# Kernel optimization log

Hardware: AMD Instinct MI355X
Metric: run time of the kernel (lower is better)

## Reference

```python
import jax, jax.numpy as jnp
import numpy as np

N, E, DIN, DH, DOUT, H, G = 50000, 640000, 128, 64, 64, 4, 16

_PARAM_SHAPES = {
    "gat1_W": (DIN, H * DH), "gat1_asrc": (H, DH), "gat1_adst": (H, DH), "gat1_b": (DH,),
    "gat2_W": (DH, H * DH), "gat2_asrc": (H, DH), "gat2_adst": (H, DH), "gat2_b": (DH,),
    "gin_W1": (DH, DH), "gin_b1": (DH,), "gin_W2": (DH, DH), "gin_b2": (DH,),
    "sage1_Wl": (DH, DH), "sage1_bl": (DH,), "sage1_Wr": (DH, DH),
    "sage2_Wl": (DH, DH), "sage2_bl": (DH,), "sage2_Wr": (DH, DH),
    "tr_Wq": (DH, H * DH), "tr_bq": (H * DH,), "tr_Wk": (DH, H * DH), "tr_bk": (H * DH,),
    "tr_Wv": (DH, H * DH), "tr_bv": (H * DH,), "tr_Ws": (DH, DH), "tr_bs": (DH,),
    "ec_W1": (2 * DH, DH), "ec_b1": (DH,), "ec_W2": (DH, DH), "ec_b2": (DH,),
    "fc1_W": (DH, DH), "fc1_b": (DH,), "fc2_W": (DH, DOUT), "fc2_b": (DOUT,),
}
_PARAM_NAMES = list(_PARAM_SHAPES)


def setup_inputs() -> dict:
    key = jax.random.key(0)
    inp = {}
    inp["x"] = jax.random.normal(jax.random.fold_in(key, 0), (N, DIN), jnp.float32)
    inp["edge_index"] = jax.random.randint(jax.random.fold_in(key, 1), (2, E), 0, N, dtype=jnp.int32)
    inp["batch"] = jnp.sort(jax.random.randint(jax.random.fold_in(key, 2), (N,), 0, G, dtype=jnp.int32))
    for i, (name, shp) in enumerate(_PARAM_SHAPES.items()):
        inp[name] = jax.random.normal(jax.random.fold_in(key, 10 + i), shp, jnp.float32) * 0.05
    return inp


def _edge_softmax(logit, dst, n):
    # softmax over incoming edges of each target node (PyG scatter-softmax)
    m = jax.ops.segment_max(logit, dst, num_segments=n)
    e = jnp.exp(logit - m[dst])
    z = jax.ops.segment_sum(e, dst, num_segments=n)
    return e / (z[dst] + 1e-16)


def _forward(x, src, dst, batch, p):
    relu = jax.nn.relu
    # GATConv adds self-loops by default
    loop = jnp.arange(N, dtype=src.dtype)
    src_sl = jnp.concatenate([src, loop])
    dst_sl = jnp.concatenate([dst, loop])

    def gat(h_in, W, a_s, a_d, b):
        h = (h_in @ W).reshape(N, H, DH)                    # [N,H,D]
        ls = jnp.einsum('nhd,hd->nh', h, a_s)
        ld = jnp.einsum('nhd,hd->nh', h, a_d)
        logit = jax.nn.leaky_relu(ls[src_sl] + ld[dst_sl], 0.2)   # [E+N,H]
        alpha = _edge_softmax(logit, dst_sl, N)
        out = jax.ops.segment_sum(h[src_sl] * alpha[:, :, None], dst_sl, num_segments=N)
        return out.mean(axis=1) + b                          # concat=False -> head mean + bias

    x1 = relu(gat(x, p["gat1_W"], p["gat1_asrc"], p["gat1_adst"], p["gat1_b"]))
    x2 = relu(gat(x1, p["gat2_W"], p["gat2_asrc"], p["gat2_adst"], p["gat2_b"]))

    # GINConv: nn((1+eps)*x + sum_j x_j), eps=0
    agg = jax.ops.segment_sum(x2[src], dst, num_segments=N)
    x3 = relu(relu((x2 + agg) @ p["gin_W1"] + p["gin_b1"]) @ p["gin_W2"] + p["gin_b2"])

    deg = jax.ops.segment_sum(jnp.ones((E,), x.dtype), dst, num_segments=N)
    deg = jnp.maximum(deg, 1.0)[:, None]

    def sage(h_in, Wl, bl, Wr):
        mean = jax.ops.segment_sum(h_in[src], dst, num_segments=N) / deg
        return mean @ Wl + bl + h_in @ Wr

    xs = relu(sage(x3, p["sage1_Wl"], p["sage1_bl"], p["sage1_Wr"]))
    x4 = relu(sage(xs, p["sage2_Wl"], p["sage2_bl"], p["sage2_Wr"]))

    # TransformerConv (heads=4, concat=False, root_weight skip)
    q = (x4 @ p["tr_Wq"] + p["tr_bq"]).reshape(N, H, DH)
    k = (x4 @ p["tr_Wk"] + p["tr_bk"]).reshape(N, H, DH)
    v = (x4 @ p["tr_Wv"] + p["tr_bv"]).reshape(N, H, DH)
    logit = (q[dst] * k[src]).sum(-1) * (1.0 / np.sqrt(DH))  # [E,H]
    alpha = _edge_softmax(logit, dst, N)
    tout = jax.ops.segment_sum(v[src] * alpha[:, :, None], dst, num_segments=N).mean(axis=1)
    x5 = relu(tout + x4 @ p["tr_Ws"] + p["tr_bs"])

    # EdgeConv: max_j nn([x_i, x_j - x_i])
    xi = x5[dst]
    feat = jnp.concatenate([xi, x5[src] - xi], axis=1)       # [E, 2*DH]
    msg = relu(feat @ p["ec_W1"] + p["ec_b1"]) @ p["ec_W2"] + p["ec_b2"]
    emax = jax.ops.segment_max(msg, dst, num_segments=N)
    x6 = relu(jnp.where(jnp.isfinite(emax), emax, 0.0))      # isolated nodes -> 0

    # global_mean_pool over batch ids
    cnt = jax.ops.segment_sum(jnp.ones((N,), x.dtype), batch, num_segments=G)
    gmean = jax.ops.segment_sum(x6, batch, num_segments=G) / jnp.maximum(cnt, 1.0)[:, None]

    # dropout layers are identity in eval mode
    return relu(gmean @ p["fc1_W"] + p["fc1_b"]) @ p["fc2_W"] + p["fc2_b"]


def reference(x, edge_index, batch,
              gat1_W, gat1_asrc, gat1_adst, gat1_b,
              gat2_W, gat2_asrc, gat2_adst, gat2_b,
              gin_W1, gin_b1, gin_W2, gin_b2,
              sage1_Wl, sage1_bl, sage1_Wr,
              sage2_Wl, sage2_bl, sage2_Wr,
              tr_Wq, tr_bq, tr_Wk, tr_bk, tr_Wv, tr_bv, tr_Ws, tr_bs,
              ec_W1, ec_b1, ec_W2, ec_b2,
              fc1_W, fc1_b, fc2_W, fc2_b):
    L = dict(locals())
    p = {n: L[n] for n in _PARAM_NAMES}
    return _forward(x, edge_index[0], edge_index[1], batch, p)
```

## Files before the change

kernel.cpp:

```cpp
#include <hip/hip_runtime.h>

#define NN 50000
#define EE 640000
#define GG 16
#define N64 (NN*64)

static inline int cdiv(int a,int b){return (a+b-1)/b;}

typedef __attribute__((ext_vector_type(8))) short bfrag;
typedef __attribute__((ext_vector_type(4))) float ffrag;

__device__ __forceinline__ float lrelu(float x){ return x>0.f? x : 0.2f*x; }
__device__ __forceinline__ unsigned fenc(float f){
  unsigned u=__float_as_uint(f);
  return (u&0x80000000u)? ~u : (u|0x80000000u);
}
__device__ __forceinline__ float bf2f(unsigned short u){ return __uint_as_float(((unsigned)u)<<16); }
__device__ __forceinline__ unsigned short f2bf(float f){
  unsigned u=__float_as_uint(f);
  u += 0x7FFFu + ((u>>16)&1u);
  return (unsigned short)(u>>16);
}

__global__ void zero_kernel(unsigned* p, int n){
  int i=blockIdx.x*blockDim.x+threadIdx.x;
  if(i<n) p[i]=0u;
}

__global__ void hist_kernel(const int* __restrict__ dst, int* __restrict__ cnt){
  int e=blockIdx.x*blockDim.x+threadIdx.x;
  if(e<EE) atomicAdd(&cnt[dst[e]],1);
}

__global__ __launch_bounds__(1024) void scan1_kernel(const int* __restrict__ cnt,
    int* __restrict__ rowptr, int* __restrict__ bsum){
  __shared__ int wsum[16];
  int t=threadIdx.x, b=blockIdx.x;
  int i=b*1024+t;
  int v=(i<NN)?cnt[i]:0;
  int lane=t&63, w=t>>6;
  int inc=v;
  #pragma unroll
  for(int o=1;o<64;o<<=1){ int u=__shfl_up(inc,o,64); if(lane>=o) inc+=u; }
  if(lane==63) wsum[w]=inc;
  __syncthreads();
  if(t<16){
    int s=wsum[t];
    #pragma unroll
    for(int o=1;o<16;o<<=1){ int u=__shfl_up(s,o,16); if(t>=o) s+=u; }
    wsum[t]=s;
  }
  __syncthreads();
  int woff=(w>0)?wsum[w-1]:0;
  if(i<NN) rowptr[i]=woff+inc-v;
  if(t==1023) bsum[b]=wsum[15];
}

__global__ void scan2_kernel(const int* __restrict__ bsum, int* __restrict__ boff, int* __restrict__ rowptr, int nb){
  int t=threadIdx.x;
  int v=(t<nb)?bsum[t]:0;
  int inc=v;
  #pragma unroll
  for(int o=1;o<64;o<<=1){ int u=__shfl_up(inc,o,64); if(t>=o) inc+=u; }
  if(t<nb) boff[t]=inc-v;
  if(t==63) rowptr[NN]=inc;
}

__global__ void scan3_kernel(int* __restrict__ rowptr, const int* __restrict__ boff,
                             const int* __restrict__ cnt, float* __restrict__ invdeg){
  int i=blockIdx.x*blockDim.x+threadIdx.x;
  if(i<NN){
    rowptr[i]+=boff[i>>10];
    invdeg[i]=1.f/fmaxf((float)cnt[i],1.f);
  }
}

__global__ void fill_kernel(const int* __restrict__ src, const int* __restrict__ dst,
                            const int* __restrict__ rowptr, int* __restrict__ fillp,
                            int* __restrict__ srcS, int* __restrict__ dstS){
  int e=blockIdx.x*blockDim.x+threadIdx.x;
  if(e>=EE) return;
  int d=dst[e];
  int p=rowptr[d]+atomicAdd(&fillp[d],1);
  srcS[p]=src[e]; dstS[p]=d;
}

__global__ void cvtx_kernel(const float* __restrict__ x, unsigned short* __restrict__ xb){
  int i=blockIdx.x*blockDim.x+threadIdx.x;
  if(i>=NN*32) return;
  float4 v=*(const float4*)(x+(size_t)i*4);
  ushort4 o; o.x=f2bf(v.x); o.y=f2bf(v.y); o.z=f2bf(v.z); o.w=f2bf(v.w);
  *(ushort4*)(xb+(size_t)i*4)=o;
}

__global__ void prep_kernel(
    const float* __restrict__ g1W, const float* __restrict__ g2W,
    const float* __restrict__ giW1, const float* __restrict__ giW2,
    const float* __restrict__ s1Wl, const float* __restrict__ s1Wr,
    const float* __restrict__ s2Wl, const float* __restrict__ s2Wr,
    const float* __restrict__ Wq, const float* __restrict__ Wk,
    const float* __restrict__ Wv, const float* __restrict__ Ws,
    const float* __restrict__ ecW1, const float* __restrict__ ecW2,
    const float* __restrict__ bq, const float* __restrict__ bk, const float* __restrict__ eb1,
    unsigned short* __restrict__ wt, float* __restrict__ bqk, float* __restrict__ bPQ){
  int i=blockIdx.x*blockDim.x+threadIdx.x;
  if(i<32768){ int n=i>>7,k=i&127; wt[i]=f2bf(g1W[k*256+n]); return; } i-=32768;
  if(i<16384){ int n=i>>6,k=i&63; wt[32768+i]=f2bf(g2W[k*256+n]); return; } i-=16384;
  if(i<4096){ int n=i>>6,k=i&63; wt[49152+i]=f2bf(giW1[k*64+n]); return; } i-=4096;
  if(i<4096){ int n=i>>6,k=i&63; wt[53248+i]=f2bf(giW2[k*64+n]); return; } i-=4096;
  if(i<8192){ int n=i>>7,k=i&127; float v=(k<64)?s1Wl[k*64+n]:s1Wr[(k-64)*64+n];
              wt[57344+i]=f2bf(v); return; } i-=8192;
  if(i<8192){ int n=i>>7,k=i&127; float v=(k<64)?s2Wl[k*64+n]:s2Wr[(k-64)*64+n];
              wt[65536+i]=f2bf(v); return; } i-=8192;
  if(i<32768){ int n=i>>6,k=i&63; float v=(n<256)?Wq[k*256+n]:Wk[k*256+(n-256)];
               wt[73728+i]=f2bf(v); return; } i-=32768;
  if(i<16384){ int n=i>>6,k=i&63; wt[106496+i]=f2bf(Wv[k*256+n]); return; } i-=16384;
  if(i<4096){ int n=i>>6,k=i&63; wt[122880+i]=f2bf(Ws[k*64+n]); return; } i-=4096;
  if(i<8192){ int n=i>>6,k=i&63;
              float v=(n<64)?(ecW1[k*64+n]-ecW1[(64+k)*64+n]):ecW1[(64+k)*64+(n-64)];
              wt[126976+i]=f2bf(v); return; } i-=8192;
  if(i<4096){ int n=i>>6,k=i&63; wt[135168+i]=f2bf(ecW2[k*64+n]); return; } i-=4096;
  if(i<640){
    if(i<256) bqk[i]=bq[i];
    else if(i<512) bqk[i]=bk[i-256];
    else { int j=i-512; bPQ[j]=(j<64)?eb1[j]:0.f; }
  }
}

template<int K>
__global__ __launch_bounds__(256) void mgemm_kernel(
    const unsigned short* __restrict__ A, const unsigned short* __restrict__ Wt,
    const float* __restrict__ bias,
    float* __restrict__ Cf, unsigned short* __restrict__ Cb, int ldc, int relu_flag,
    const float* __restrict__ a_s, const float* __restrict__ a_d,
    float* __restrict__ lsO, float* __restrict__ ldO){
  __shared__ float lsP[2][4][64];
  const int m0=blockIdx.x*64;
  const int tid=threadIdx.x;
  const int w=tid>>6, l=tid&63, lo=l&15, quad=l>>4;
  const int colg=blockIdx.y*64 + w*16 + lo;
  const unsigned short* wrow=Wt+(size_t)colg*K+quad*8;
  ffrag acc[4];
  #pragma unroll
  for(int t=0;t<4;t++) acc[t]=(ffrag){0.f,0.f,0.f,0.f};
  int rows[4];
  #pragma unroll
  for(int t=0;t<4;t++){ int r=m0+t*16+lo; rows[t]=(r<NN)?r:(NN-1); }
  #pragma unroll
  for(int kc=0;kc<K;kc+=32){
    bfrag b=*(const bfrag*)(wrow+kc);
    #pragma unroll
    for(int t=0;t<4;t++){
      bfrag a=*(const bfrag*)(A+(size_t)rows[t]*K+kc+quad*8);
      acc[t]=__builtin_amdgcn_mfma_f32_16x16x32_bf16(a,b,acc[t],0,0,0);
    }
  }
  float bv=bias?bias[colg]:0.f;
  float asv=0.f,adv=0.f;
  if(lsO){ asv=a_s[colg]; adv=a_d[colg]; }
  #pragma unroll
  for(int t=0;t<4;t++){
    #pragma unroll
    for(int r=0;r<4;r++){
      float v=acc[t][r]+bv;
      if(relu_flag) v=fmaxf(v,0.f);
      int row=m0+t*16+quad*4+r;
      if(row<NN){
        if(Cb) Cb[(size_t)row*ldc+colg]=f2bf(v);
        else   Cf[(size_t)row*ldc+colg]=v;
      }
      if(lsO){
        float ps=v*asv, pd=v*adv;
        #pragma unroll
        for(int o=1;o<16;o<<=1){ ps+=__shfl_xor(ps,o,16); pd+=__shfl_xor(pd,o,16); }
        if(lo==0){ int lr=t*16+quad*4+r; lsP[0][w][lr]=ps; lsP[1][w][lr]=pd; }
      }
    }
  }
  if(lsO){
    __syncthreads();
    if(tid<64){
      int row=m0+tid;
      if(row<NN){
        lsO[(size_t)row*4+blockIdx.y]=lsP[0][0][tid]+lsP[0][1][tid]+lsP[0][2][tid]+lsP[0][3][tid];
        ldO[(size_t)row*4+blockIdx.y]=lsP[1][0][tid]+lsP[1][1][tid]+lsP[1][2][tid]+lsP[1][3][tid];
      }
    }
  }
}

__global__ void gat_exp_kernel(const int* __restrict__ srcS, const int* __restrict__ dstS,
    const float* __restrict__ ls4, const float* __restrict__ ld4, float* __restrict__ eE){
  int j=blockIdx.x*blockDim.x+threadIdx.x;
  if(j>=EE) return;
  int s=srcS[j], d=dstS[j];
  const float4 a=*(const float4*)(ls4+(size_t)4*s);
  const float4 b=*(const float4*)(ld4+(size_t)4*d);
  *(float4*)(eE+(size_t)4*j)=make_float4(
    __expf(lrelu(a.x+b.x)),__expf(lrelu(a.y+b.y)),
    __expf(lrelu(a.z+b.z)),__expf(lrelu(a.w+b.w)));
}

__global__ __launch_bounds__(256) void gat1p_kernel(const unsigned short* __restrict__ h,
    const int* __restrict__ rowptr, const int* __restrict__ srcS,
    const float* __restrict__ eE,
    const float* __restrict__ ls4, const float* __restrict__ ld4,
    const float* __restrict__ bias, unsigned short* __restrict__ outb){
  __shared__ float cz[4][4];
  __shared__ float ca[4][4][64];
  int w=threadIdx.x>>6, lane=threadIdx.x&63;
  int n=blockIdx.x*2+(w>>1);
  int half=w&1;
  float z0=0.f,z1=0.f,z2=0.f,z3=0.f;
  float a0=0.f,a1=0.f,a2=0.f,a3=0.f;
  if(n<NN){
    int r0=rowptr[n], r1=rowptr[n+1];
    int mid=(r0+r1)>>1;
    if(half==0){
      const float4 ldv=*(const float4*)(ld4+(size_t)4*n);
      const float4 lsv=*(const float4*)(ls4+(size_t)4*n);
      z0=__expf(lrelu(lsv.x+ldv.x)); z1=__expf(lrelu(lsv.y+ldv.y));
      z2=__expf(lrelu(lsv.z+ldv.z)); z3=__expf(lrelu(lsv.w+ldv.w));
      const unsigned short* hn=h+(size_t)n*256;
      a0=z0*bf2f(hn[lane]); a1=z1*bf2f(hn[64+lane]);
      a2=z2*bf2f(hn[128+lane]); a3=z3*bf2f(hn[192+lane]);
    }
    int j = half? mid : r0;
    int je= half? r1  : mid;
    for(; j+3<je; j+=4){
      int s0=srcS[j], s1=srcS[j+1], s2=srcS[j+2], s3=srcS[j+3];
      const float4 E0=*(const float4*)(eE+(size_t)4*j);
      const float4 E1=*(const float4*)(eE+(size_t)4*(j+1));
      const float4 E2=*(const float4*)(eE+(size_t)4*(j+2));
      const float4 E3=*(const float4*)(eE+(size_t)4*(j+3));
      const unsigned short* h0=h+(size_t)s0*256;
      const unsigned short* h1=h+(size_t)s1*256;
      const unsigned short* h2=h+(size_t)s2*256;
      const unsigned short* h3=h+(size_t)s3*256;
      z0+=(E0.x+E1.x)+(E2.x+E3.x); z1+=(E0.y+E1.y)+(E2.y+E3.y);
      z2+=(E0.z+E1.z)+(E2.z+E3.z); z3+=(E0.w+E1.w)+(E2.w+E3.w);
      a0+=(E0.x*bf2f(h0[lane])+E1.x*bf2f(h1[lane]))+(E2.x*bf2f(h2[lane])+E3.x*bf2f(h3[lane]));
      a1+=(E0.y*bf2f(h0[64+lane])+E1.y*bf2f(h1[64+lane]))+(E2.y*bf2f(h2[64+lane])+E3.y*bf2f(h3[64+lane]));
      a2+=(E0.z*bf2f(h0[128+lane])+E1.z*bf2f(h1[128+lane]))+(E2.z*bf2f(h2[128+lane])+E3.z*bf2f(h3[128+lane]));
      a3+=(E0.w*bf2f(h0[192+lane])+E1.w*bf2f(h1[192+lane]))+(E2.w*bf2f(h2[192+lane])+E3.w*bf2f(h3[192+lane]));
    }
    for(; j<je; j++){
      int s0=srcS[j];
      const float4 E0=*(const float4*)(eE+(size_t)4*j);
      const unsigned short* h0=h+(size_t)s0*256;
      z0+=E0.x; z1+=E0.y; z2+=E0.z; z3+=E0.w;
      a0+=E0.x*bf2f(h0[lane]); a1+=E0.y*bf2f(h0[64+lane]);
      a2+=E0.z*bf2f(h0[128+lane]); a3+=E0.w*bf2f(h0[192+lane]);
    }
  }
  if(lane==0){ cz[w][0]=z0; cz[w][1]=z1; cz[w][2]=z2; cz[w][3]=z3; }
  ca[w][0][lane]=a0; ca[w][1][lane]=a1; ca[w][2][lane]=a2; ca[w][3][lane]=a3;
  __syncthreads();
  if(threadIdx.x<128){
    int ni=threadIdx.x>>6, l=threadIdx.x&63;
    int n2=blockIdx.x*2+ni;
    if(n2<NN){
      int w0=ni*2, w1=w0+1;
      float Z0=cz[w0][0]+cz[w1][0], Z1=cz[w0][1]+cz[w1][1];
      float Z2=cz[w0][2]+cz[w1][2], Z3=cz[w0][3]+cz[w1][3];
      float A0=ca[w0][0][l]+ca[w1][0][l], A1=ca[w0][1][l]+ca[w1][1][l];
      float A2=ca[w0][2][l]+ca[w1][2][l], A3=ca[w0][3][l]+ca[w1][3][l];
      float r=0.25f*(A0/(Z0+1e-16f)+A1/(Z1+1e-16f)+A2/(Z2+1e-16f)+A3/(Z3+1e-16f))+bias[l];
      outb[(size_t)n2*64+l]=f2bf(fmaxf(r,0.f));
    }
  }
}

__global__ __launch_bounds__(256) void agg_kernel(const unsigned short* __restrict__ xin,
    const int* __restrict__ rowptr, const int* __restrict__ srcS,
    unsigned short* __restrict__ out){
  int n=blockIdx.x*4+(threadIdx.x>>6);
  int lane=threadIdx.x&63;
  if(n>=NN) return;
  int r0=rowptr[n], r1=rowptr[n+1];
  float acc=bf2f(xin[(size_t)n*64+lane]);
  int j=r0;
  for(; j+3<r1; j+=4){
    int s0=srcS[j], s1=srcS[j+1], s2=srcS[j+2], s3=srcS[j+3];
    acc+=(bf2f(xin[(size_t)s0*64+lane])+bf2f(xin[(size_t)s1*64+lane]))
        +(bf2f(xin[(size_t)s2*64+lane])+bf2f(xin[(size_t)s3*64+lane]));
  }
  for(; j<r1; j++) acc+=bf2f(xin[(size_t)srcS[j]*64+lane]);
  out[(size_t)n*64+lane]=f2bf(acc);
}

__global__ __launch_bounds__(256) void agg2_kernel(const unsigned short* __restrict__ xin,
    const int* __restrict__ rowptr, const int* __restrict__ srcS,
    const float* __restrict__ invdeg, unsigned short* __restrict__ out128b){
  int n=blockIdx.x*4+(threadIdx.x>>6);
  int lane=threadIdx.x&63;
  if(n>=NN) return;
  int r0=rowptr[n], r1=rowptr[n+1];
  float acc=0.f;
  int j=r0;
  for(; j+3<r1; j+=4){
    int s0=srcS[j], s1=srcS[j+1], s2=srcS[j+2], s3=srcS[j+3];
    acc+=(bf2f(xin[(size_t)s0*64+lane])+bf2f(xin[(size_t)s1*64+lane]))
        +(bf2f(xin[(size_t)s2*64+lane])+bf2f(xin[(size_t)s3*64+lane]));
  }
  for(; j<r1; j++) acc+=bf2f(xin[(size_t)srcS[j]*64+lane]);
  out128b[(size_t)n*128+lane]=f2bf(acc*invdeg[n]);
  out128b[(size_t)n*128+64+lane]=xin[(size_t)n*64+lane];
}

__global__ __launch_bounds__(256) void tr_pass1_kernel(const int* __restrict__ srcS, const int* __restrict__ dstS,
    const unsigned short* __restrict__ qk, float* __restrict__ lg){
  int e=blockIdx.x*16+(threadIdx.x>>4);
  int t=threadIdx.x&15;
  if(e>=EE) return;
  int s=srcS[e], d=dstS[e];
  const unsigned short* qd=qk+(size_t)d*512+t*4;
  const unsigned short* ks=qk+(size_t)s*512+256+t*4;
  ushort4 ku0=*(const ushort4*)(ks);
  ushort4 ku1=*(const ushort4*)(ks+64);
  ushort4 ku2=*(const ushort4*)(ks+128);
  ushort4 ku3=*(const ushort4*)(ks+192);
  ushort4 qu0=*(const ushort4*)(qd);
  ushort4 qu1=*(const ushort4*)(qd+64);
  ushort4 qu2=*(const ushort4*)(qd+128);
  ushort4 qu3=*(const ushort4*)(qd+192);
  float v0=bf2f(ku0.x)*bf2f(qu0.x)+bf2f(ku0.y)*bf2f(qu0.y)+bf2f(ku0.z)*bf2f(qu0.z)+bf2f(ku0.w)*bf2f(qu0.w);
  float v1=bf2f(ku1.x)*bf2f(qu1.x)+bf2f(ku1.y)*bf2f(qu1.y)+bf2f(ku1.z)*bf2f(qu1.z)+bf2f(ku1.w)*bf2f(qu1.w);
  float v2=bf2f(ku2.x)*bf2f(qu2.x)+bf2f(ku2.y)*bf2f(qu2.y)+bf2f(ku2.z)*bf2f(qu2.z)+bf2f(ku2.w)*bf2f(qu2.w);
  float v3=bf2f(ku3.x)*bf2f(qu3.x)+bf2f(ku3.y)*bf2f(qu3.y)+bf2f(ku3.z)*bf2f(qu3.z)+bf2f(ku3.w)*bf2f(qu3.w);
  #pragma unroll
  for(int o=1;o<16;o<<=1){
    v0+=__shfl_xor(v0,o,16); v1+=__shfl_xor(v1,o,16);
    v2+=__shfl_xor(v2,o,16); v3+=__shfl_xor(v3,o,16);
  }
  if(t==0)
    *(float4*)(lg+(size_t)4*e)=make_float4(__expf(v0*0.125f),__expf(v1*0.125f),
                                           __expf(v2*0.125f),__expf(v3*0.125f));
}

__global__ __launch_bounds__(256) void tr_pass2_kernel(const int* __restrict__ rowptr, const int* __restrict__ srcS,
    const float* __restrict__ lg,
    const unsigned short* __restrict__ v, const float* __restrict__ skip, unsigned short* __restrict__ x5b){
  __shared__ float cz[4][4];
  __shared__ float ca[4][4][64];
  int w=threadIdx.x>>6, lane=threadIdx.x&63;
  int n=blockIdx.x*2+(w>>1);
  int half=w&1;
  float z0=0.f,z1=0.f,z2=0.f,z3=0.f;
  float a0=0.f,a1=0.f,a2=0.f,a3=0.f;
  if(n<NN){
    int r0=rowptr[n], r1=rowptr[n+1];
    int mid=(r0+r1)>>1;
    int j = half? mid : r0;
    int je= half? r1  : mid;
    for(; j+3<je; j+=4){
      int s0=srcS[j], s1=srcS[j+1], s2=srcS[j+2], s3=srcS[j+3];
      const float4 E0=*(const float4*)(lg+(size_t)4*j);
      const float4 E1=*(const float4*)(lg+(size_t)4*(j+1));
      const float4 E2=*(const float4*)(lg+(size_t)4*(j+2));
      const float4 E3=*(const float4*)(lg+(size_t)4*(j+3));
      const unsigned short* v0=v+(size_t)s0*256;
      const unsigned short* v1=v+(size_t)s1*256;
      const unsigned short* v2=v+(size_t)s2*256;
      const unsigned short* v3=v+(size_t)s3*256;
      z0+=(E0.x+E1.x)+(E2.x+E3.x); z1+=(E0.y+E1.y)+(E2.y+E3.y);
      z2+=(E0.z+E1.z)+(E2.z+E3.z); z3+=(E0.w+E1.w)+(E2.w+E3.w);
      a0+=(E0.x*bf2f(v0[lane])+E1.x*bf2f(v1[lane]))+(E2.x*bf2f(v2[lane])+E3.x*bf2f(v3[lane]));
      a1+=(E0.y*bf2f(v0[64+lane])+E1.y*bf2f(v1[64+lane]))+(E2.y*bf2f(v2[64+lane])+E3.y*bf2f(v3[64+lane]));
      a2+=(E0.z*bf2f(v0[128+lane])+E1.z*bf2f(v1[128+lane]))+(E2.z*bf2f(v2[128+lane])+E3.z*bf2f(v3[128+lane]));
      a3+=(E0.w*bf2f(v0[192+lane])+E1.w*bf2f(v1[192+lane]))+(E2.w*bf2f(v2[192+lane])+E3.w*bf2f(v3[192+lane]));
    }
    for(; j<je; j++){
      int s0=srcS[j];
      const float4 E0=*(const float4*)(lg+(size_t)4*j);
      const unsigned short* v0=v+(size_t)s0*256;
      z0+=E0.x; z1+=E0.y; z2+=E0.z; z3+=E0.w;
      a0+=E0.x*bf2f(v0[lane]); a1+=E0.y*bf2f(v0[64+lane]);
      a2+=E0.z*bf2f(v0[128+lane]); a3+=E0.w*bf2f(v0[192+lane]);
    }
  }
  if(lane==0){ cz[w][0]=z0; cz[w][1]=z1; cz[w][2]=z2; cz[w][3]=z3; }
  ca[w][0][lane]=a0; ca[w][1][lane]=a1; ca[w][2][lane]=a2; ca[w][3][lane]=a3;
  __syncthreads();
  if(threadIdx.x<128){
    int ni=threadIdx.x>>6, l=threadIdx.x&63;
    int n2=blockIdx.x*2+ni;
    if(n2<NN){
      int w0=ni*2, w1=w0+1;
      float Z0=cz[w0][0]+cz[w1][0], Z1=cz[w0][1]+cz[w1][1];
      float Z2=cz[w0][2]+cz[w1][2], Z3=cz[w0][3]+cz[w1][3];
      float A0=ca[w0][0][l]+ca[w1][0][l], A1=ca[w0][1][l]+ca[w1][1][l];
      float A2=ca[w0][2][l]+ca[w1][2][l], A3=ca[w0][3][l]+ca[w1][3][l];
      float t=0.25f*(A0/(Z0+1e-16f)+A1/(Z1+1e-16f)+A2/(Z2+1e-16f)+A3/(Z3+1e-16f))+skip[(size_t)n2*64+l];
      x5b[(size_t)n2*64+l]=f2bf(fmaxf(t,0.f));
    }
  }
}

__global__ __launch_bounds__(256) void edgeconv3_kernel(
    const unsigned short* __restrict__ PQ,
    const int* __restrict__ srcS, const int* __restrict__ dstS,
    const unsigned short* __restrict__ W2t, const float* __restrict__ b2,
    unsigned* __restrict__ emax){
  __shared__ unsigned short Hs[64][72];
  __shared__ float As[64][66];
  __shared__ int dstL[64];
  const int e0=blockIdx.x*64;
  const int tid=threadIdx.x;
  if(tid<64) dstL[tid]=dstS[e0+tid];
  #pragma unroll
  for(int it=0;it<4;it++){
    int linear=it*1024+tid*4;
    int m=linear>>6, k=linear&63;
    int e=e0+m;
    int dn=dstS[e], sn=srcS[e];
    ushort4 pu=*(const ushort4*)(PQ+(size_t)dn*128+k);
    ushort4 qu=*(const ushort4*)(PQ+(size_t)sn*128+64+k);
    ushort4 hh;
    hh.x=f2bf(fmaxf(bf2f(pu.x)+bf2f(qu.x),0.f));
    hh.y=f2bf(fmaxf(bf2f(pu.y)+bf2f(qu.y),0.f));
    hh.z=f2bf(fmaxf(bf2f(pu.z)+bf2f(qu.z),0.f));
    hh.w=f2bf(fmaxf(bf2f(pu.w)+bf2f(qu.w),0.f));
    *(ushort4*)&Hs[m][k]=hh;
  }
  __syncthreads();
  const int w=tid>>6, l=tid&63, lo=l&15, quad=l>>4;
  const int colg=w*16+lo;
  ffrag acc[4];
  #pragma unroll
  for(int t=0;t<4;t++) acc[t]=(ffrag){0.f,0.f,0.f,0.f};
  #pragma unroll
  for(int kc=0;kc<64;kc+=32){
    bfrag b=*(const bfrag*)(W2t+(size_t)colg*64+kc+quad*8);
    #pragma unroll
    for(int t=0;t<4;t++){
      bfrag a=*(const bfrag*)(&Hs[t*16+lo][kc+quad*8]);
      acc[t]=__builtin_amdgcn_mfma_f32_16x16x32_bf16(a,b,acc[t],0,0,0);
    }
  }
  float bv=b2[colg];
  #pragma unroll
  for(int t=0;t<4;t++)
    #pragma unroll
    for(int r=0;r<4;r++)
      As[t*16+quad*4+r][colg]=acc[t][r]+bv;
  __syncthreads();
  if(tid<64){
    const int c=tid;
    const int dFirst=dstL[0], dLast=dstL[63];
    int dprev=dFirst;
    float mx=As[0][c];
    #pragma unroll 8
    for(int m=1;m<64;m++){
      int dn=dstL[m];
      float v=As[m][c];
      if(dn!=dprev){
        unsigned* addr=&emax[(size_t)dprev*64+c];
        unsigned enc=fenc(mx);
        if(dprev!=dFirst && dprev!=dLast) *addr=enc;
        else atomicMax(addr,enc);
        dprev=dn; mx=v;
      }else mx=fmaxf(mx,v);
    }
    unsigned* addr=&emax[(size_t)dprev*64+c];
    unsigned enc=fenc(mx);
    if(dprev!=dFirst && dprev!=dLast) *addr=enc;
    else atomicMax(addr,enc);
  }
}

__global__ __launch_bounds__(256) void pool_kernel(const unsigned* __restrict__ emax, const int* __restrict__ batch,
                                                   float* __restrict__ pooled){
  const int NB=200;
  int base=blockIdx.x*NB;
  int lane=threadIdx.x&63;
  int wsub=threadIdx.x>>6;
  float acc=0.f; int curg=-1;
  for(int idx=wsub; idx<NB; idx+=4){
    int n=base+idx;
    if(n>=NN) break;
    int g=batch[n];
    if(g!=curg){
      if(curg>=0) atomicAdd(&pooled[curg*64+lane],acc);
      acc=0.f; curg=g;
    }
    unsigned u=emax[(size_t)n*64+lane];
    acc+=(u>=0x80000000u)? __uint_as_float(u&0x7fffffffu) : 0.f;
  }
  if(curg>=0) atomicAdd(&pooled[curg*64+lane],acc);
}

__global__ __launch_bounds__(256) void final_kernel(const float* __restrict__ pooled, const int* __restrict__ batch,
    const float* __restrict__ fc1W, const float* __restrict__ fc1b,
    const float* __restrict__ fc2W, const float* __restrict__ fc2b,
    float* __restrict__ out){
  __shared__ float gm[16][64];
  __shared__ float t1[16][64];
  __shared__ int cgs[17];
  int t=threadIdx.x;
  if(t<17){
    int lo=0, hi=NN;
    while(lo<hi){ int mid=(lo+hi)>>1; if(batch[mid]<t) lo=mid+1; else hi=mid; }
    cgs[t]=lo;
  }
  __syncthreads();
  for(int r=0;r<4;r++){
    int idx=r*256+t; int g=idx>>6, d=idx&63;
    float c=(float)(cgs[g+1]-cgs[g]);
    gm[g][d]=pooled[idx]/fmaxf(c,1.f);
  }
  __syncthreads();
  for(int r=0;r<4;r++){
    int idx=r*256+t; int g=idx>>6, d=idx&63;
    float a=fc1b[d];
    for(int k2=0;k2<64;k2++) a+=gm[g][k2]*fc1W[k2*64+d];
    t1[g][d]=fmaxf(a,0.f);
  }
  __syncthreads();
  for(int r=0;r<4;r++){
    int idx=r*256+t; int g=idx>>6, d=idx&63;
    float a=fc2b[d];
    for(int k2=0;k2<64;k2++) a+=t1[g][k2]*fc2W[k2*64+d];
    out[idx]=a;
  }
}

extern "C" void kernel_launch(void* const* d_in, const int* in_sizes, int n_in,
                              void* d_out, int out_size, void* d_ws, size_t ws_size,
                              hipStream_t stream){
  const float* x       =(const float*)d_in[0];
  const int*   ei      =(const int*)  d_in[1];
  const int*   src     =ei;
  const int*   dst     =ei+EE;
  const int*   batch   =(const int*)  d_in[2];
  const float* gat1_W  =(const float*)d_in[3];
  const float* gat1_as =(const float*)d_in[4];
  const float* gat1_ad =(const float*)d_in[5];
  const float* gat1_b  =(const float*)d_in[6];
  const float* gat2_W  =(const float*)d_in[7];
  const float* gat2_as =(const float*)d_in[8];
  const float* gat2_ad =(const float*)d_in[9];
  const float* gat2_b  =(const float*)d_in[10];
  const float* gin_W1  =(const float*)d_in[11];
  const float* gin_b1  =(const float*)d_in[12];
  const float* gin_W2  =(const float*)d_in[13];
  const float* gin_b2  =(const float*)d_in[14];
  const float* sage1_Wl=(const float*)d_in[15];
  const float* sage1_bl=(const float*)d_in[16];
  const float* sage1_Wr=(const float*)d_in[17];
  const float* sage2_Wl=(const float*)d_in[18];
  const float* sage2_bl=(const float*)d_in[19];
  const float* sage2_Wr=(const float*)d_in[20];
  const float* tr_Wq   =(const float*)d_in[21];
  const float* tr_bq   =(const float*)d_in[22];
  const float* tr_Wk   =(const float*)d_in[23];
  const float* tr_bk   =(const float*)d_in[24];
  const float* tr_Wv   =(const float*)d_in[25];
  const float* tr_bv   =(const float*)d_in[26];
  const float* tr_Ws   =(const float*)d_in[27];
  const float* tr_bs   =(const float*)d_in[28];
  const float* ec_W1   =(const float*)d_in[29];
  const float* ec_b1   =(const float*)d_in[30];
  const float* ec_W2   =(const float*)d_in[31];
  const float* ec_b2   =(const float*)d_in[32];
  const float* fc1_W   =(const float*)d_in[33];
  const float* fc1_b   =(const float*)d_in[34];
  const float* fc2_W   =(const float*)d_in[35];
  const float* fc2_b   =(const float*)d_in[36];

  float* base=(float*)d_ws;
  size_t off=0;
  auto alloc=[&](size_t n){ float* p=base+off; off+=n; return p; };
  float* A_big =alloc((size_t)NN*256);
  float* nb0   =alloc(N64);
  float* nb1   =alloc(N64);
  float* nb2   =alloc(N64);
  float* nb3   =alloc(N64);
  float* nb4   =alloc(N64);
  float* nb5   =alloc(N64);
  float* logitE=alloc((size_t)EE*4);
  float* ls    =alloc(NN*4);
  float* ldb   =alloc(NN*4);
  float* invdeg=alloc(NN);
  float* pooled=alloc(GG*64);
  float* wbuf  =alloc(70000);
  float* bbuf  =alloc(640);
  int* ibase=(int*)(base+off);
  int* srcS  =ibase;
  int* dstS  =ibase+EE;
  int* cnt   =ibase+2*EE;
  int* fillp =ibase+2*EE+NN;
  int* rowptr=ibase+2*EE+2*NN;
  int* bsum  =ibase+2*EE+3*NN+8;
  int* boff  =bsum+64;

  const int BT=256;
  const int NSB=cdiv(NN,1024);
  zero_kernel<<<cdiv(2*NN,BT),BT,0,stream>>>((unsigned*)cnt,2*NN);
  zero_kernel<<<cdiv(GG*64,BT),BT,0,stream>>>((unsigned*)pooled,GG*64);
  zero_kernel<<<cdiv(N64,BT),BT,0,stream>>>((unsigned*)nb5,N64);
  hist_kernel<<<cdiv(EE,BT),BT,0,stream>>>(dst,cnt);
  scan1_kernel<<<NSB,1024,0,stream>>>(cnt,rowptr,bsum);
  scan2_kernel<<<1,64,0,stream>>>(bsum,boff,rowptr,NSB);
  scan3_kernel<<<cdiv(NN,BT),BT,0,stream>>>(rowptr,boff,cnt,invdeg);
  fill_kernel<<<cdiv(EE,BT),BT,0,stream>>>(src,dst,rowptr,fillp,srcS,dstS);

  const int GB=cdiv(NN,64);
  const int GW=cdiv(NN,4);
  const int GW2=cdiv(NN,2);

  unsigned short* wt =(unsigned short*)wbuf;
  float* bqk=bbuf;
  float* bPQ=bbuf+512;
  unsigned short* hbf  =(unsigned short*)A_big;
  unsigned short* xb   =(unsigned short*)A_big+(size_t)NN*256;
  unsigned short* xcatb=(unsigned short*)A_big;
  unsigned short* qkb  =(unsigned short*)A_big;
  unsigned short* x1b  =(unsigned short*)nb0;
  unsigned short* x2b  =(unsigned short*)nb1;
  unsigned short* tb   =(unsigned short*)nb2;
  unsigned short* hb3  =(unsigned short*)nb3;
  unsigned short* x3b  =(unsigned short*)nb1;
  unsigned short* xsb  =(unsigned short*)nb2;
  unsigned short* x4b  =(unsigned short*)nb0;
  unsigned short* vb   =(unsigned short*)nb1;
  unsigned short* x5b  =(unsigned short*)nb4;
  float* skipf=nb3;
  unsigned short* PQb  =(unsigned short*)nb1;

  prep_kernel<<<cdiv(139904,BT),BT,0,stream>>>(gat1_W,gat2_W,gin_W1,gin_W2,
      sage1_Wl,sage1_Wr,sage2_Wl,sage2_Wr,tr_Wq,tr_Wk,tr_Wv,tr_Ws,ec_W1,ec_W2,
      tr_bq,tr_bk,ec_b1,wt,bqk,bPQ);
  cvtx_kernel<<<cdiv(NN*32,BT),BT,0,stream>>>(x,xb);

  mgemm_kernel<128><<<dim3(GB,4),BT,0,stream>>>(xb,wt,nullptr,nullptr,hbf,256,0,
                                                gat1_as,gat1_ad,ls,ldb);
  gat_exp_kernel<<<cdiv(EE,BT),BT,0,stream>>>(srcS,dstS,ls,ldb,logitE);
  gat1p_kernel<<<GW2,BT,0,stream>>>(hbf,rowptr,srcS,logitE,ls,ldb,gat1_b,x1b);
  mgemm_kernel<64><<<dim3(GB,4),BT,0,stream>>>(x1b,wt+32768,nullptr,nullptr,hbf,256,0,
                                               gat2_as,gat2_ad,ls,ldb);
  gat_exp_kernel<<<cdiv(EE,BT),BT,0,stream>>>(srcS,dstS,ls,ldb,logitE);
  gat1p_kernel<<<GW2,BT,0,stream>>>(hbf,rowptr,srcS,logitE,ls,ldb,gat2_b,x2b);
  agg_kernel<<<GW,BT,0,stream>>>(x2b,rowptr,srcS,tb);
  mgemm_kernel<64><<<dim3(GB,1),BT,0,stream>>>(tb,wt+49152,gin_b1,nullptr,hb3,64,1,
                                               nullptr,nullptr,nullptr,nullptr);
  mgemm_kernel<64><<<dim3(GB,1),BT,0,stream>>>(hb3,wt+53248,gin_b2,nullptr,x3b,64,1,
                                               nullptr,nullptr,nullptr,nullptr);
  agg2_kernel<<<GW,BT,0,stream>>>(x3b,rowptr,srcS,invdeg,xcatb);
  mgemm_kernel<128><<<dim3(GB,1),BT,0,stream>>>(xcatb,wt+57344,sage1_bl,nullptr,xsb,64,1,
                                                nullptr,nullptr,nullptr,nullptr);
  agg2_kernel<<<GW,BT,0,stream>>>(xsb,rowptr,srcS,invdeg,xcatb);
  mgemm_kernel<128><<<dim3(GB,1),BT,0,stream>>>(xcatb,wt+65536,sage2_bl,nullptr,x4b,64,1,
                                                nullptr,nullptr,nullptr,nullptr);
  mgemm_kernel<64><<<dim3(GB,8),BT,0,stream>>>(x4b,wt+73728,bqk,nullptr,qkb,512,0,
                                               nullptr,nullptr,nullptr,nullptr);
  tr_pass1_kernel<<<cdiv(EE,16),BT,0,stream>>>(srcS,dstS,qkb,logitE);
  mgemm_kernel<64><<<dim3(GB,4),BT,0,stream>>>(x4b,wt+106496,tr_bv,nullptr,vb,256,0,
                                               nullptr,nullptr,nullptr,nullptr);
  mgemm_kernel<64><<<dim3(GB,1),BT,0,stream>>>(x4b,wt+122880,tr_bs,skipf,nullptr,64,0,
                                               nullptr,nullptr,nullptr,nullptr);
  tr_pass2_kernel<<<GW2,BT,0,stream>>>(rowptr,srcS,logitE,vb,skipf,x5b);
  mgemm_kernel<64><<<dim3(GB,2),BT,0,stream>>>(x5b,wt+126976,bPQ,nullptr,PQb,128,0,
                                               nullptr,nullptr,nullptr,nullptr);
  edgeconv3_kernel<<<EE/64,BT,0,stream>>>(PQb,srcS,dstS,wt+135168,ec_b2,(unsigned*)nb5);
  pool_kernel<<<cdiv(NN,200),BT,0,stream>>>((unsigned*)nb5,batch,pooled);
  final_kernel<<<1,BT,0,stream>>>(pooled,batch,fc1_W,fc1_b,fc2_W,fc2_b,(float*)d_out);
}
```

Before: 854.2 us.

## Store GAT and transformer gather features in FP8 and fuse edge-exp into aggregation

The GAT h, transformer Q/K and V projections are now written as FP8 (e4m3) bytes, and head-interleaved where needed, so each gather in the aggregation kernels reads 4 bytes per lane instead of four scattered bf16 loads. The separate gat_exp kernel is removed, and gat1p recomputes exp(leaky_relu(ls[src]+ld[dst])) inline, which saves a per-edge logit write and read. The cost is much lower feature precision, with a risk of exceeding tolerance, plus extra exp work inside the aggregation loop.

Result: faster. 821.4 us (-3.8%).

```diff
diff --git a/kernel.cpp b/kernel.cpp
--- a/kernel.cpp
+++ b/kernel.cpp
@@ -9,6 +9,7 @@
 
 typedef __attribute__((ext_vector_type(8))) short bfrag;
 typedef __attribute__((ext_vector_type(4))) float ffrag;
+typedef __attribute__((ext_vector_type(2))) float f32x2;
 
 __device__ __forceinline__ float lrelu(float x){ return x>0.f? x : 0.2f*x; }
 __device__ __forceinline__ unsigned fenc(float f){
@@ -20,6 +21,21 @@
   unsigned u=__float_as_uint(f);
   u += 0x7FFFu + ((u>>16)&1u);
   return (unsigned short)(u>>16);
+}
+__device__ __forceinline__ unsigned char f2f8(float f){
+  return (unsigned char)(__builtin_amdgcn_cvt_pk_fp8_f32(f,f,0,false)&0xff);
+}
+__device__ __forceinline__ void f8x4(unsigned u, float& e0,float& e1,float& e2,float& e3){
+  f32x2 lo=__builtin_amdgcn_cvt_pk_f32_fp8((int)u,false);
+  f32x2 hi=__builtin_amdgcn_cvt_pk_f32_fp8((int)u,true);
+  e0=lo.x; e1=lo.y; e2=hi.x; e3=hi.y;
+}
+__device__ __forceinline__ float dot4f8(unsigned a, unsigned b){
+  f32x2 al=__builtin_amdgcn_cvt_pk_f32_fp8((int)a,false);
+  f32x2 ah=__builtin_amdgcn_cvt_pk_f32_fp8((int)a,true);
+  f32x2 bl=__builtin_amdgcn_cvt_pk_f32_fp8((int)b,false);
+  f32x2 bh=__builtin_amdgcn_cvt_pk_f32_fp8((int)b,true);
+  return al.x*bl.x+al.y*bl.y+ah.x*bh.x+ah.y*bh.y;
 }
 
 __global__ void zero_kernel(unsigned* p, int n){
@@ -131,7 +147,8 @@
 __global__ __launch_bounds__(256) void mgemm_kernel(
     const unsigned short* __restrict__ A, const unsigned short* __restrict__ Wt,
     const float* __restrict__ bias,
-    float* __restrict__ Cf, unsigned short* __restrict__ Cb, int ldc, int relu_flag,
+    float* __restrict__ Cf, unsigned short* __restrict__ Cb, unsigned char* __restrict__ C8,
+    int ldc, int relu_flag, int c8dh,
     const float* __restrict__ a_s, const float* __restrict__ a_d,
     float* __restrict__ lsO, float* __restrict__ ldO){
   __shared__ float lsP[2][4][64];
@@ -166,7 +183,8 @@
       if(relu_flag) v=fmaxf(v,0.f);
       int row=m0+t*16+quad*4+r;
       if(row<NN){
-        if(Cb) Cb[(size_t)row*ldc+colg]=f2bf(v);
+        if(C8){ int ci=c8dh?(((colg&63)<<2)|(colg>>6)):colg; C8[(size_t)row*ldc+ci]=f2f8(v); }
+        else if(Cb) Cb[(size_t)row*ldc+colg]=f2bf(v);
         else   Cf[(size_t)row*ldc+colg]=v;
       }
       if(lsO){
@@ -189,21 +207,8 @@
   }
 }
 
-__global__ void gat_exp_kernel(const int* __restrict__ srcS, const int* __restrict__ dstS,
-    const float* __restrict__ ls4, const float* __restrict__ ld4, float* __restrict__ eE){
-  int j=blockIdx.x*blockDim.x+threadIdx.x;
-  if(j>=EE) return;
-  int s=srcS[j], d=dstS[j];
-  const float4 a=*(const float4*)(ls4+(size_t)4*s);
-  const float4 b=*(const float4*)(ld4+(size_t)4*d);
-  *(float4*)(eE+(size_t)4*j)=make_float4(
-    __expf(lrelu(a.x+b.x)),__expf(lrelu(a.y+b.y)),
-    __expf(lrelu(a.z+b.z)),__expf(lrelu(a.w+b.w)));
-}
-
-__global__ __launch_bounds__(256) void gat1p_kernel(const unsigned short* __restrict__ h,
+__global__ __launch_bounds__(256) void gat1p_kernel(const unsigned char* __restrict__ h8,
     const int* __restrict__ rowptr, const int* __restrict__ srcS,
-    const float* __restrict__ eE,
     const float* __restrict__ ls4, const float* __restrict__ ld4,
     const float* __restrict__ bias, unsigned short* __restrict__ outb){
   __shared__ float cz[4][4];
@@ -214,43 +219,57 @@
   float z0=0.f,z1=0.f,z2=0.f,z3=0.f;
   float a0=0.f,a1=0.f,a2=0.f,a3=0.f;
   if(n<NN){
+    const float4 ldv=*(const float4*)(ld4+(size_t)4*n);
     int r0=rowptr[n], r1=rowptr[n+1];
     int mid=(r0+r1)>>1;
     if(half==0){
-      const float4 ldv=*(const float4*)(ld4+(size_t)4*n);
       const float4 lsv=*(const float4*)(ls4+(size_t)4*n);
       z0=__expf(lrelu(lsv.x+ldv.x)); z1=__expf(lrelu(lsv.y+ldv.y));
       z2=__expf(lrelu(lsv.z+ldv.z)); z3=__expf(lrelu(lsv.w+ldv.w));
-      const unsigned short* hn=h+(size_t)n*256;
-      a0=z0*bf2f(hn[lane]); a1=z1*bf2f(hn[64+lane]);
-      a2=z2*bf2f(hn[128+lane]); a3=z3*bf2f(hn[192+lane]);
+      float h0,h1,h2,h3;
+      f8x4(*(const unsigned*)(h8+(size_t)n*256+lane*4),h0,h1,h2,h3);
+      a0=z0*h0; a1=z1*h1; a2=z2*h2; a3=z3*h3;
     }
     int j = half? mid : r0;
     int je= half? r1  : mid;
     for(; j+3<je; j+=4){
       int s0=srcS[j], s1=srcS[j+1], s2=srcS[j+2], s3=srcS[j+3];
-      const float4 E0=*(const float4*)(eE+(size_t)4*j);
-      const float4 E1=*(const float4*)(eE+(size_t)4*(j+1));
-      const float4 E2=*(const float4*)(eE+(size_t)4*(j+2));
-      const float4 E3=*(const float4*)(eE+(size_t)4*(j+3));
-      const unsigned short* h0=h+(size_t)s0*256;
-      const unsigned short* h1=h+(size_t)s1*256;
-      const unsigned short* h2=h+(size_t)s2*256;
-      const unsigned short* h3=h+(size_t)s3*256;
-      z0+=(E0.x+E1.x)+(E2.x+E3.x); z1+=(E0.y+E1.y)+(E2.y+E3.y);
-      z2+=(E0.z+E1.z)+(E2.z+E3.z); z3+=(E0.w+E1.w)+(E2.w+E3.w);
-      a0+=(E0.x*bf2f(h0[lane])+E1.x*bf2f(h1[lane]))+(E2.x*bf2f(h2[lane])+E3.x*bf2f(h3[lane]));
-      a1+=(E0.y*bf2f(h0[64+lane])+E1.y*bf2f(h1[64+lane]))+(E2.y*bf2f(h2[64+lane])+E3.y*bf2f(h3[64+lane]));
-      a2+=(E0.z*bf2f(h0[128+lane])+E1.z*bf2f(h1[128+lane]))+(E2.z*bf2f(h2[128+lane])+E3.z*bf2f(h3[128+lane]));
-      a3+=(E0.w*bf2f(h0[192+lane])+E1.w*bf2f(h1[192+lane]))+(E2.w*bf2f(h2[192+lane])+E3.w*bf2f(h3[192+lane]));
+      float4 L0=*(const float4*)(ls4+(size_t)4*s0);
+      float4 L1=*(const float4*)(ls4+(size_t)4*s1);
+      float4 L2=*(const float4*)(ls4+(size_t)4*s2);
+      float4 L3=*(const float4*)(ls4+(size_t)4*s3);
+      unsigned u0=*(const unsigned*)(h8+(size_t)s0*256+lane*4);
+      unsigned u1=*(const unsigned*)(h8+(size_t)s1*256+lane*4);
+      unsigned u2=*(const unsigned*)(h8+(size_t)s2*256+lane*4);
+      unsigned u3=*(const unsigned*)(h8+(size_t)s3*256+lane*4);
+      float E0x=__expf(lrelu(L0.x+ldv.x)),E0y=__expf(lrelu(L0.y+ldv.y)),
+            E0z=__expf(lrelu(L0.z+ldv.z)),E0w=__expf(lrelu(L0.w+ldv.w));
+      float E1x=__expf(lrelu(L1.x+ldv.x)),E1y=__expf(lrelu(L1.y+ldv.y)),
+            E1z=__expf(lrelu(L1.z+ldv.z)),E1w=__expf(lrelu(L1.w+ldv.w));
+      float E2x=__expf(lrelu(L2.x+ldv.x)),E2y=__expf(lrelu(L2.y+ldv.y)),
+            E2z=__expf(lrelu(L2.z+ldv.z)),E2w=__expf(lrelu(L2.w+ldv.w));
+      float E3x=__expf(lrelu(L3.x+ldv.x)),E3y=__expf(lrelu(L3.y+ldv.y)),
+            E3z=__expf(lrelu(L3.z+ldv.z)),E3w=__expf(lrelu(L3.w+ldv.w));
+      float h00,h01,h02,h03; f8x4(u0,h00,h01,h02,h03);
+      float h10,h11,h12,h13; f8x4(u1,h10,h11,h12,h13);
+      float h20,h21,h22,h23; f8x4(u2,h20,h21,h22,h23);
+      float h30,h31,h32,h33; f8x4(u3,h30,h31,h32,h33);
+      z0+=(E0x+E1x)+(E2x+E3x); z1+=(E0y+E1y)+(E2y+E3y);
+      z2+=(E0z+E1z)+(E2z+E3z); z3+=(E0w+E1w)+(E2w+E3w);
+      a0+=(E0x*h00+E1x*h10)+(E2x*h20+E3x*h30);
+      a1+=(E0y*h01+E1y*h11)+(E2y*h21+E3y*h31);
+      a2+=(E0z*h02+E1z*h12)+(E2z*h22+E3z*h32);
+      a3+=(E0w*h03+E1w*h13)+(E2w*h23+E3w*h33);
     }
     for(; j<je; j++){
       int s0=srcS[j];
-      const float4 E0=*(const float4*)(eE+(size_t)4*j);
-      const unsigned short* h0=h+(size_t)s0*256;
-      z0+=E0.x; z1+=E0.y; z2+=E0.z; z3+=E0.w;
-      a0+=E0.x*bf2f(h0[lane]); a1+=E0.y*bf2f(h0[64+lane]);
-      a2+=E0.z*bf2f(h0[128+lane]); a3+=E0.w*bf2f(h0[192+lane]);
+      float4 L0=*(const float4*)(ls4+(size_t)4*s0);
+      unsigned u0=*(const unsigned*)(h8+(size_t)s0*256+lane*4);
+      float E0x=__expf(lrelu(L0.x+ldv.x)),E0y=__expf(lrelu(L0.y+ldv.y)),
+            E0z=__expf(lrelu(L0.z+ldv.z)),E0w=__expf(lrelu(L0.w+ldv.w));
+      float h00,h01,h02,h03; f8x4(u0,h00,h01,h02,h03);
+      z0+=E0x; z1+=E0y; z2+=E0z; z3+=E0w;
+      a0+=E0x*h00; a1+=E0y*h01; a2+=E0z*h02; a3+=E0w*h03;
     }
   }
   if(lane==0){ cz[w][0]=z0; cz[w][1]=z1; cz[w][2]=z2; cz[w][3]=z3; }
@@ -309,25 +328,25 @@
 }
 
 __global__ __launch_bounds__(256) void tr_pass1_kernel(const int* __restrict__ srcS, const int* __restrict__ dstS,
-    const unsigned short* __restrict__ qk, float* __restrict__ lg){
+    const unsigned char* __restrict__ qk8, float* __restrict__ lg){
   int e=blockIdx.x*16+(threadIdx.x>>4);
   int t=threadIdx.x&15;
   if(e>=EE) return;
   int s=srcS[e], d=dstS[e];
-  const unsigned short* qd=qk+(size_t)d*512+t*4;
-  const unsigned short* ks=qk+(size_t)s*512+256+t*4;
-  ushort4 ku0=*(const ushort4*)(ks);
-  ushort4 ku1=*(const ushort4*)(ks+64);
-  ushort4 ku2=*(const ushort4*)(ks+128);
-  ushort4 ku3=*(const ushort4*)(ks+192);
-  ushort4 qu0=*(const ushort4*)(qd);
-  ushort4 qu1=*(const ushort4*)(qd+64);
-  ushort4 qu2=*(const ushort4*)(qd+128);
-  ushort4 qu3=*(const ushort4*)(qd+192);
-  float v0=bf2f(ku0.x)*bf2f(qu0.x)+bf2f(ku0.y)*bf2f(qu0.y)+bf2f(ku0.z)*bf2f(qu0.z)+bf2f(ku0.w)*bf2f(qu0.w);
-  float v1=bf2f(ku1.x)*bf2f(qu1.x)+bf2f(ku1.y)*bf2f(qu1.y)+bf2f(ku1.z)*bf2f(qu1.z)+bf2f(ku1.w)*bf2f(qu1.w);
-  float v2=bf2f(ku2.x)*bf2f(qu2.x)+bf2f(ku2.y)*bf2f(qu2.y)+bf2f(ku2.z)*bf2f(qu2.z)+bf2f(ku2.w)*bf2f(qu2.w);
-  float v3=bf2f(ku3.x)*bf2f(qu3.x)+bf2f(ku3.y)*bf2f(qu3.y)+bf2f(ku3.z)*bf2f(qu3.z)+bf2f(ku3.w)*bf2f(qu3.w);
+  const unsigned char* qd=qk8+(size_t)d*512+t*4;
+  const unsigned char* ks=qk8+(size_t)s*512+256+t*4;
+  unsigned ku0=*(const unsigned*)(ks);
+  unsigned ku1=*(const unsigned*)(ks+64);
+  unsigned ku2=*(const unsigned*)(ks+128);
+  unsigned ku3=*(const unsigned*)(ks+192);
+  unsigned qu0=*(const unsigned*)(qd);
+  unsigned qu1=*(const unsigned*)(qd+64);
+  unsigned qu2=*(const unsigned*)(qd+128);
+  unsigned qu3=*(const unsigned*)(qd+192);
+  float v0=dot4f8(ku0,qu0);
+  float v1=dot4f8(ku1,qu1);
+  float v2=dot4f8(ku2,qu2);
+  float v3=dot4f8(ku3,qu3);
   #pragma unroll
   for(int o=1;o<16;o<<=1){
     v0+=__shfl_xor(v0,o,16); v1+=__shfl_xor(v1,o,16);
@@ -340,7 +359,7 @@
 
 __global__ __launch_bounds__(256) void tr_pass2_kernel(const int* __restrict__ rowptr, const int* __restrict__ srcS,
     const float* __restrict__ lg,
-    const unsigned short* __restrict__ v, const float* __restrict__ skip, unsigned short* __restrict__ x5b){
+    const unsigned char* __restrict__ v8, const float* __restrict__ skip, unsigned short* __restrict__ x5b){
   __shared__ float cz[4][4];
   __shared__ float ca[4][4][64];
   int w=threadIdx.x>>6, lane=threadIdx.x&63;
@@ -359,24 +378,28 @@
       const float4 E1=*(const float4*)(lg+(size_t)4*(j+1));
       const float4 E2=*(const float4*)(lg+(size_t)4*(j+2));
       const float4 E3=*(const float4*)(lg+(size_t)4*(j+3));
-      const unsigned short* v0=v+(size_t)s0*256;
-      const unsigned short* v1=v+(size_t)s1*256;
-      const unsigned short* v2=v+(size_t)s2*256;
-      const unsigned short* v3=v+(size_t)s3*256;
+      unsigned u0=*(const unsigned*)(v8+(size_t)s0*256+lane*4);
+      unsigned u1=*(const unsigned*)(v8+(size_t)s1*256+lane*4);
+      unsigned u2=*(const unsigned*)(v8+(size_t)s2*256+lane*4);
+      unsigned u3=*(const unsigned*)(v8+(size_t)s3*256+lane*4);
+      float h00,h01,h02,h03; f8x4(u0,h00,h01,h02,h03);
+      float h10,h11,h12,h13; f8x4(u1,h10,h11,h12,h13);
+      float h20,h21,h22,h23; f8x4(u2,h20,h21,h22,h23);
+      float h30,h31,h32,h33; f8x4(u3,h30,h31,h32,h33);
       z0+=(E0.x+E1.x)+(E2.x+E3.x); z1+=(E0.y+E1.y)+(E2.y+E3.y);
       z2+=(E0.z+E1.z)+(E2.z+E3.z); z3+=(E0.w+E1.w)+(E2.w+E3.w);
-      a0+=(E0.x*bf2f(v0[lane])+E1.x*bf2f(v1[lane]))+(E2.x*bf2f(v2[lane])+E3.x*bf2f(v3[lane]));
-      a1+=(E0.y*bf2f(v0[64+lane])+E1.y*bf2f(v1[64+lane]))+(E2.y*bf2f(v2[64+lane])+E3.y*bf2f(v3[64+lane]));
-      a2+=(E0.z*bf2f(v0[128+lane])+E1.z*bf2f(v1[128+lane]))+(E2.z*bf2f(v2[128+lane])+E3.z*bf2f(v3[128+lane]));
-      a3+=(E0.w*bf2f(v0[192+lane])+E1.w*bf2f(v1[192+lane]))+(E2.w*bf2f(v2[192+lane])+E3.w*bf2f(v3[192+lane]));
+      a0+=(E0.x*h00+E1.x*h10)+(E2.x*h20+E3.x*h30);
+      a1+=(E0.y*h01+E1.y*h11)+(E2.y*h21+E3.y*h31);
+      a2+=(E0.z*h02+E1.z*h12)+(E2.z*h22+E3.z*h32);
+      a3+=(E0.w*h03+E1.w*h13)+(E2.w*h23+E3.w*h33);
     }
     for(; j<je; j++){
       int s0=srcS[j];
       const float4 E0=*(const float4*)(lg+(size_t)4*j);
-      const unsigned short* v0=v+(size_t)s0*256;
+      unsigned u0=*(const unsigned*)(v8+(size_t)s0*256+lane*4);
+      float h00,h01,h02,h03; f8x4(u0,h00,h01,h02,h03);
       z0+=E0.x; z1+=E0.y; z2+=E0.z; z3+=E0.w;
-      a0+=E0.x*bf2f(v0[lane]); a1+=E0.y*bf2f(v0[64+lane]);
-      a2+=E0.z*bf2f(v0[128+lane]); a3+=E0.w*bf2f(v0[192+lane]);
+      a0+=E0.x*h00; a1+=E0.y*h01; a2+=E0.z*h02; a3+=E0.w*h03;
     }
   }
   if(lane==0){ cz[w][0]=z0; cz[w][1]=z1; cz[w][2]=z2; cz[w][3]=z3; }
@@ -612,10 +635,10 @@
   unsigned short* wt =(unsigned short*)wbuf;
   float* bqk=bbuf;
   float* bPQ=bbuf+512;
-  unsigned short* hbf  =(unsigned short*)A_big;
+  unsigned char*  h8   =(unsigned char*)A_big;
+  unsigned char*  qk8  =(unsigned char*)A_big;
   unsigned short* xb   =(unsigned short*)A_big+(size_t)NN*256;
   unsigned short* xcatb=(unsigned short*)A_big;
-  unsigned short* qkb  =(unsigned short*)A_big;
   unsigned short* x1b  =(unsigned short*)nb0;
   unsigned short* x2b  =(unsigned short*)nb1;
   unsigned short* tb   =(unsigned short*)nb2;
@@ -623,7 +646,7 @@
   unsigned short* x3b  =(unsigned short*)nb1;
   unsigned short* xsb  =(unsigned short*)nb2;
   unsigned short* x4b  =(unsigned short*)nb0;
-  unsigned short* vb   =(unsigned short*)nb1;
+  unsigned char*  v8   =(unsigned char*)nb1;
   unsigned short* x5b  =(unsigned short*)nb4;
   float* skipf=nb3;
   unsigned short* PQb  =(unsigned short*)nb1;
@@ -633,34 +656,32 @@
       tr_bq,tr_bk,ec_b1,wt,bqk,bPQ);
   cvtx_kernel<<<cdiv(NN*32,BT),BT,0,stream>>>(x,xb);
 
-  mgemm_kernel<128><<<dim3(GB,4),BT,0,stream>>>(xb,wt,nullptr,nullptr,hbf,256,0,
+  mgemm_kernel<128><<<dim3(GB,4),BT,0,stream>>>(xb,wt,nullptr,nullptr,nullptr,h8,256,0,1,
                                                 gat1_as,gat1_ad,ls,ldb);
-  gat_exp_kernel<<<cdiv(EE,BT),BT,0,stream>>>(srcS,dstS,ls,ldb,logitE);
-  gat1p_kernel<<<GW2,BT,0,stream>>>(hbf,rowptr,srcS,logitE,ls,ldb,gat1_b,x1b);
-  mgemm_kernel<64><<<dim3(GB,4),BT,0,stream>>>(x1b,wt+32768,nullptr,nullptr,hbf,256,0,
+  gat1p_kernel<<<GW2,BT,0,stream>>>(h8,rowptr,srcS,ls,ldb,gat1_b,x1b);
+  mgemm_kernel<64><<<dim3(GB,4),BT,0,stream>>>(x1b,wt+32768,nullptr,nullptr,nullptr,h8,256,0,1,
                                                gat2_as,gat2_ad,ls,ldb);
-  gat_exp_kernel<<<cdiv(EE,BT),BT,0,stream>>>(srcS,dstS,ls,ldb,logitE);
-  gat1p_kernel<<<GW2,BT,0,stream>>>(hbf,rowptr,srcS,logitE,ls,ldb,gat2_b,x2b);
+  gat1p_kernel<<<GW2,BT,0,stream>>>(h8,rowptr,srcS,ls,ldb,gat2_b,x2b);
   agg_kernel<<<GW,BT,0,stream>>>(x2b,rowptr,srcS,tb);
-  mgemm_kernel<64><<<dim3(GB,1),BT,0,stream>>>(tb,wt+49152,gin_b1,nullptr,hb3,64,1,
+  mgemm_kernel<64><<<dim3(GB,1),BT,0,stream>>>(tb,wt+49152,gin_b1,nullptr,hb3,nullptr,64,1,0,
                                                nullptr,nullptr,nullptr,nullptr);
-  mgemm_kernel<64><<<dim3(GB,1),BT,0,stream>>>(hb3,wt+53248,gin_b2,nullptr,x3b,64,1,
+  mgemm_kernel<64><<<dim3(GB,1),BT,0,stream>>>(hb3,wt+53248,gin_b2,nullptr,x3b,nullptr,64,1,0,
                                                nullptr,nullptr,nullptr,nullptr);
   agg2_kernel<<<GW,BT,0,stream>>>(x3b,rowptr,srcS,invdeg,xcatb);
-  mgemm_kernel<128><<<dim3(GB,1),BT,0,stream>>>(xcatb,wt+57344,sage1_bl,nullptr,xsb,64,1,
+  mgemm_kernel<128><<<dim3(GB,1),BT,0,stream>>>(xcatb,wt+57344,sage1_bl,nullptr,xsb,nullptr,64,1,0,
                                                 nullptr,nullptr,nullptr,nullptr);
   agg2_kernel<<<GW,BT,0,stream>>>(xsb,rowptr,srcS,invdeg,xcatb);
-  mgemm_kernel<128><<<dim3(GB,1),BT,0,stream>>>(xcatb,wt+65536,sage2_bl,nullptr,x4b,64,1,
+  mgemm_kernel<128><<<dim3(GB,1),BT,0,stream>>>(xcatb,wt+65536,sage2_bl,nullptr,x4b,nullptr,64,1,0,
                                                 nullptr,nullptr,nullptr,nullptr);
-  mgemm_kernel<64><<<dim3(GB,8),BT,0,stream>>>(x4b,wt+73728,bqk,nullptr,qkb,512,0,
+  mgemm_kernel<64><<<dim3(GB,8),BT,0,stream>>>(x4b,wt+73728,bqk,nullptr,nullptr,qk8,512,0,0,
                                                nullptr,nullptr,nullptr,nullptr);
-  tr_pass1_kernel<<<cdiv(EE,16),BT,0,stream>>>(srcS,dstS,qkb,logitE);
-  mgemm_kernel<64><<<dim3(GB,4),BT,0,stream>>>(x4b,wt+106496,tr_bv,nullptr,vb,256,0,
+  tr_pass1_kernel<<<cdiv(EE,16),BT,0,stream>>>(srcS,dstS,qk8,logitE);
+  mgemm_kernel<64><<<dim3(GB,4),BT,0,stream>>>(x4b,wt+106496,tr_bv,nullptr,nullptr,v8,256,0,1,
                                                nullptr,nullptr,nullptr,nullptr);
-  mgemm_kernel<64><<<dim3(GB,1),BT,0,stream>>>(x4b,wt+122880,tr_bs,skipf,nullptr,64,0,
+  mgemm_kernel<64><<<dim3(GB,1),BT,0,stream>>>(x4b,wt+122880,tr_bs,skipf,nullptr,nullptr,64,0,0,
                                                nullptr,nullptr,nullptr,nullptr);
-  tr_pass2_kernel<<<GW2,BT,0,stream>>>(rowptr,srcS,logitE,vb,skipf,x5b);
-  mgemm_kernel<64><<<dim3(GB,2),BT,0,stream>>>(x5b,wt+126976,bPQ,nullptr,PQb,128,0,
+  tr_pass2_kernel<<<GW2,BT,0,stream>>>(rowptr,srcS,logitE,v8,skipf,x5b);
+  mgemm_kernel<64><<<dim3(GB,2),BT,0,stream>>>(x5b,wt+126976,bPQ,nullptr,PQb,nullptr,128,0,0,
                                                nullptr,nullptr,nullptr,nullptr);
   edgeconv3_kernel<<<EE/64,BT,0,stream>>>(PQb,srcS,dstS,wt+135168,ec_b2,(unsigned*)nb5);
   pool_kernel<<<cdiv(NN,200),BT,0,stream>>>((unsigned*)nb5,batch,pooled);
```
